# Performance work log

Measured on AMD Instinct MI355X. Metric: run time of the kernel, lower is better.

## Reference

```python
import jax, jax.numpy as jnp
import numpy as np

D_MODEL = 512
N_HEADS = 8
B, T = 2, 2048
EPS = 1e-6


def _phi(x):
    # ELU feature map: elu(x) + 1 (always positive)
    return jax.nn.elu(x) + 1.0


def setup_inputs() -> dict:
    key = jax.random.key(0)
    ks = jax.random.split(key, 9)
    s = 1.0 / np.sqrt(D_MODEL)
    x = jax.random.normal(ks[0], (B, T, D_MODEL), dtype=jnp.float32)
    Wq = jax.random.uniform(ks[1], (D_MODEL, D_MODEL), jnp.float32, -s, s)
    bq = jax.random.uniform(ks[2], (D_MODEL,), jnp.float32, -s, s)
    Wk = jax.random.uniform(ks[3], (D_MODEL, D_MODEL), jnp.float32, -s, s)
    bk = jax.random.uniform(ks[4], (D_MODEL,), jnp.float32, -s, s)
    Wv = jax.random.uniform(ks[5], (D_MODEL, D_MODEL), jnp.float32, -s, s)
    bv = jax.random.uniform(ks[6], (D_MODEL,), jnp.float32, -s, s)
    Wo = jax.random.uniform(ks[7], (D_MODEL, D_MODEL), jnp.float32, -s, s)
    bo = jax.random.uniform(ks[8], (D_MODEL,), jnp.float32, -s, s)
    return {"x": x, "Wq": Wq, "bq": bq, "Wk": Wk, "bk": bk,
            "Wv": Wv, "bv": bv, "Wo": Wo, "bo": bo}


def reference(x, Wq, bq, Wk, bk, Wv, bv, Wo, bo):
    Bb, Tt, _ = x.shape
    H = N_HEADS
    D = D_MODEL // H

    def heads(W, b):
        # (B,T,d_model) -> (B,H,T,D)
        return (x @ W + b).reshape(Bb, Tt, H, D).transpose(0, 2, 1, 3)

    Q = _phi(heads(Wq, bq))
    K = _phi(heads(Wk, bk))
    V = heads(Wv, bv)

    # Causal linear attention: S_t = sum_{j<=t} phi(K_j) ⊗ V_j, z_t = sum_{j<=t} phi(K_j)
    KV = jnp.einsum('bhtd,bhtm->bhtdm', K, V)   # (B,H,T,D,D)
    S = jnp.cumsum(KV, axis=2)
    z = jnp.cumsum(K, axis=2)
    num = jnp.einsum('bhtd,bhtdm->bhtm', Q, S)  # (B,H,T,D)
    den = jnp.maximum(jnp.einsum('bhtd,bhtd->bht', Q, z), EPS)[..., None]
    out = num / den

    out = out.transpose(0, 2, 1, 3).reshape(Bb, Tt, D_MODEL)
    return out @ Wo + bo
```

## Files before the change

### kernel.cpp

```cpp
#include <hip/hip_runtime.h>
#include <math.h>

#define DM 512
#define NH 8
#define HD 64
#define BB 2
#define TT 2048
#define CHUNK 64
#define NC (TT / CHUNK)
#define BH (BB * NH)
#define ROWS (BB * TT)
#define EPSV 1e-6f

typedef short bf16x8 __attribute__((ext_vector_type(8)));
typedef float f32x4 __attribute__((ext_vector_type(4)));
typedef unsigned short us;

union U4 { us h[4]; uint2 u; };

__device__ __forceinline__ us f2bf(float f) {
    unsigned int u = __float_as_uint(f);
    return (us)((u + 0x7FFFu + ((u >> 16) & 1u)) >> 16);
}
__device__ __forceinline__ float bf2f(us h) {
    return __uint_as_float(((unsigned int)h) << 16);
}
__device__ __forceinline__ void gload16(const void* g, void* l) {
    __builtin_amdgcn_global_load_lds(
        (const __attribute__((address_space(1))) unsigned int*)g,
        (__attribute__((address_space(3))) unsigned int*)l, 16, 0, 0);
}
#define SWZ(r, k) ((k) ^ (((r) & 7) << 3))

__global__ __launch_bounds__(256) void prep(
    const float* __restrict__ x,
    const float* __restrict__ Wq, const float* __restrict__ Wk,
    const float* __restrict__ Wv, const float* __restrict__ Wo,
    us* __restrict__ xb, us* __restrict__ WT)
{
    const int bid = blockIdx.x, tid = threadIdx.x;
    __shared__ float tl[32][33];
    if (bid < 2048) {
        const int i = bid * 256 + tid;
        float4 v = ((const float4*)x)[i];
        U4 o;
        o.h[0] = f2bf(v.x); o.h[1] = f2bf(v.y);
        o.h[2] = f2bf(v.z); o.h[3] = f2bf(v.w);
        ((uint2*)xb)[i] = o.u;
    } else {
        const int b2 = bid - 2048;
        const int which = b2 >> 8, t = b2 & 255;
        const float* W = (which == 0) ? Wq : (which == 1) ? Wk : (which == 2) ? Wv : Wo;
        us* O = WT + (size_t)which * DM * DM;
        const int r0 = (t >> 4) * 32, c0 = (t & 15) * 32;
        const int tr = tid >> 3, tc = tid & 7;
        float4 v = *(const float4*)&W[(size_t)(r0 + tr) * DM + c0 + tc * 4];
        tl[tr][tc * 4 + 0] = v.x; tl[tr][tc * 4 + 1] = v.y;
        tl[tr][tc * 4 + 2] = v.z; tl[tr][tc * 4 + 3] = v.w;
        __syncthreads();
        U4 o;
#pragma unroll
        for (int i = 0; i < 4; ++i) o.h[i] = f2bf(tl[tc * 4 + i][tr]);
        *(uint2*)&O[(size_t)(c0 + tr) * DM + r0 + tc * 4] = o.u;
    }
}

__device__ __forceinline__ void gemm64x128(
    const us* __restrict__ Ag, const us* __restrict__ Bg,
    int r0, int c0, int tid, us* Asl, us* Bsl, f32x4 (&acc)[2][4])
{
    const int lane = tid & 63, wid = tid >> 6;
    const int wr = wid >> 1, wc = wid & 1;
    const int lrow = lane & 15, lk8 = (lane >> 4) * 8;
    const int fa = tid * 8;

    for (int k0 = 0; k0 < DM; k0 += 64) {
        __syncthreads();
#pragma unroll
        for (int i = 0; i < 2; ++i) {
            const int f = fa + i * 2048, row = f >> 6, kp = f & 63;
            gload16(Ag + (size_t)(r0 + row) * DM + k0 + SWZ(row, kp), Asl + f);
        }
#pragma unroll
        for (int i = 0; i < 4; ++i) {
            const int f = fa + i * 2048, row = f >> 6, kp = f & 63;
            gload16(Bg + (size_t)(c0 + row) * DM + k0 + SWZ(row, kp), Bsl + f);
        }
        __syncthreads();
#pragma unroll
        for (int kin = 0; kin < 64; kin += 32) {
            bf16x8 af[2], bfr[4];
#pragma unroll
            for (int mi = 0; mi < 2; ++mi) {
                const int row = wr * 32 + mi * 16 + lrow;
                af[mi] = *(const bf16x8*)&Asl[row * 64 + SWZ(row, kin + lk8)];
            }
#pragma unroll
            for (int ni = 0; ni < 4; ++ni) {
                const int row = wc * 64 + ni * 16 + lrow;
                bfr[ni] = *(const bf16x8*)&Bsl[row * 64 + SWZ(row, kin + lk8)];
            }
#pragma unroll
            for (int mi = 0; mi < 2; ++mi)
#pragma unroll
                for (int ni = 0; ni < 4; ++ni)
                    acc[mi][ni] = __builtin_amdgcn_mfma_f32_16x16x32_bf16(
                        af[mi], bfr[ni], acc[mi][ni], 0, 0, 0);
        }
    }
}

__global__ __launch_bounds__(256) void qkv_mfma(
    const us* __restrict__ xb, const us* __restrict__ WT,
    const float* __restrict__ bq, const float* __restrict__ bk,
    const float* __restrict__ bv,
    us* __restrict__ qn, us* __restrict__ kn,
    us* __restrict__ kt, us* __restrict__ vt)
{
    const int which = blockIdx.z;
    const us* Bg = WT + (size_t)which * DM * DM;
    const float* bias = (which == 0) ? bq : (which == 1) ? bk : bv;

    __shared__ us Asl[64 * 64];
    __shared__ us Bsl[128 * 64];
    f32x4 acc[2][4] = {};
    const int r0 = blockIdx.x * 64, c0 = blockIdx.y * 128;
    const int tid = threadIdx.x;

    gemm64x128(xb, Bg, r0, c0, tid, Asl, Bsl, acc);

    const int lane = tid & 63, wid = tid >> 6;
    const int wr = wid >> 1, wc = wid & 1;
    const int lrow = lane & 15, lr4 = (lane >> 4) * 4;
    const int b = r0 >> 11;

#pragma unroll
    for (int mi = 0; mi < 2; ++mi) {
        const int rowb = r0 + wr * 32 + mi * 16 + lr4;
        const int t0g = rowb & (TT - 1);
#pragma unroll
        for (int ni = 0; ni < 4; ++ni) {
            const int col = c0 + wc * 64 + ni * 16 + lrow;
            const int h = col >> 6, d = col & 63;
            const float bc = bias[col];
            U4 p4;
#pragma unroll
            for (int r = 0; r < 4; ++r) {
                float y = acc[mi][ni][r] + bc;
                if (which < 2) y = (y > 0.f) ? (y + 1.f) : __expf(y);
                const us hb = f2bf(y);
                p4.h[r] = hb;
                if (which == 0)
                    qn[((size_t)(b * NH + h) * TT + t0g + r) * HD + d] = hb;
                else if (which == 1)
                    kn[((size_t)(b * NH + h) * TT + t0g + r) * HD + d] = hb;
            }
            if (which == 1)
                *(uint2*)&kt[((size_t)(b * NH + h) * HD + d) * TT + t0g] = p4.u;
            else if (which == 2)
                *(uint2*)&vt[((size_t)(b * NH + h) * HD + d) * TT + t0g] = p4.u;
        }
    }
}

__global__ __launch_bounds__(256) void out_mfma(
    const us* __restrict__ Ag, const us* __restrict__ WoT,
    const float* __restrict__ bias, float* __restrict__ out)
{
    __shared__ us Asl[64 * 64];
    __shared__ us Bsl[128 * 64];
    f32x4 acc[2][4] = {};
    const int r0 = blockIdx.x * 64, c0 = blockIdx.y * 128;
    const int tid = threadIdx.x;

    gemm64x128(Ag, WoT, r0, c0, tid, Asl, Bsl, acc);

    const int lane = tid & 63, wid = tid >> 6;
    const int wr = wid >> 1, wc = wid & 1;
    const int lrow = lane & 15, lr4 = (lane >> 4) * 4;

#pragma unroll
    for (int mi = 0; mi < 2; ++mi)
#pragma unroll
        for (int ni = 0; ni < 4; ++ni) {
            const int col = c0 + wc * 64 + ni * 16 + lrow;
            const float bc = bias[col];
#pragma unroll
            for (int r = 0; r < 4; ++r) {
                const int row = r0 + wr * 32 + mi * 16 + lr4 + r;
                out[(size_t)row * DM + col] = acc[mi][ni][r] + bc;
            }
        }
}

__global__ __launch_bounds__(256) void chunk_sums(
    const us* __restrict__ kt, const us* __restrict__ vt,
    us* __restrict__ kvc, float* __restrict__ zc)
{
    const int blk = blockIdx.x, bh = blk >> 5, c = blk & 31;
    const int t0 = c * CHUNK;
    __shared__ us Ksl[4096], Vsl[4096];
    __shared__ float partial[4][64];
    const int tid = threadIdx.x;
    const us* ktb = kt + (size_t)bh * HD * TT;
    const us* vtb = vt + (size_t)bh * HD * TT;

#pragma unroll
    for (int i = 0; i < 2; ++i) {
        const int f = tid * 8 + i * 2048, row = f >> 6, kp = f & 63;
        const int kl = SWZ(row, kp);
        gload16(ktb + (size_t)row * TT + t0 + kl, Ksl + f);
        gload16(vtb + (size_t)row * TT + t0 + kl, Vsl + f);
    }
    __syncthreads();

    const int lane = tid & 63, wid = tid >> 6;
    const int wr = wid >> 1, wc = wid & 1;
    const int lrow = lane & 15, lk8 = (lane >> 4) * 8, lr4 = (lane >> 4) * 4;

    f32x4 acc[2][2] = {};
#pragma unroll
    for (int kin = 0; kin < 64; kin += 32) {
        bf16x8 af[2], bfr[2];
#pragma unroll
        for (int mi = 0; mi < 2; ++mi) {
            const int row = wr * 32 + mi * 16 + lrow;
            af[mi] = *(const bf16x8*)&Vsl[row * 64 + SWZ(row, kin + lk8)];
        }
#pragma unroll
        for (int ni = 0; ni < 2; ++ni) {
            const int row = wc * 32 + ni * 16 + lrow;
            bfr[ni] = *(const bf16x8*)&Ksl[row * 64 + SWZ(row, kin + lk8)];
        }
#pragma unroll
        for (int mi = 0; mi < 2; ++mi)
#pragma unroll
            for (int ni = 0; ni < 2; ++ni)
                acc[mi][ni] = __builtin_amdgcn_mfma_f32_16x16x32_bf16(
                    af[mi], bfr[ni], acc[mi][ni], 0, 0, 0);
    }

    us* dst = kvc + (size_t)blk * 4096;
#pragma unroll
    for (int mi = 0; mi < 2; ++mi)
#pragma unroll
        for (int ni = 0; ni < 2; ++ni) {
            const int d2 = wr * 32 + mi * 16 + lr4;
            const int d1 = wc * 32 + ni * 16 + lrow;
#pragma unroll
            for (int r = 0; r < 4; ++r)
                dst[(d2 + r) * 64 + d1] = f2bf(acc[mi][ni][r]);
        }

    {
        const int p = tid >> 6, d = tid & 63;
        float s = 0.f;
#pragma unroll
        for (int j = 0; j < 16; ++j)
            s += bf2f(Ksl[d * 64 + SWZ(d, p * 16 + j)]);
        partial[p][d] = s;
    }
    __syncthreads();
    if (tid < 64)
        zc[(size_t)blk * 64 + tid] =
            partial[0][tid] + partial[1][tid] + partial[2][tid] + partial[3][tid];
}

__global__ __launch_bounds__(256) void scan(
    const us* __restrict__ kvc, const float* __restrict__ zc,
    us* __restrict__ spr, float* __restrict__ zpr)
{
    const int bh = blockIdx.x, seg = blockIdx.y, tid = threadIdx.x;
    if (seg < 8) {
        const int e = seg * 512 + tid * 2;
        float r0 = 0.f, r1 = 0.f;
        for (int c = 0; c < NC; ++c) {
            const size_t off = (size_t)(bh * NC + c) * 4096 + e;
            const unsigned u = *(const unsigned*)(kvc + off);
            const unsigned p = (unsigned)f2bf(r0) | ((unsigned)f2bf(r1) << 16);
            *(unsigned*)(spr + off) = p;
            r0 += bf2f((us)(u & 0xFFFF));
            r1 += bf2f((us)(u >> 16));
        }
    } else if (tid < 64) {
        float run = 0.f;
        for (int c = 0; c < NC; ++c) {
            const size_t off = (size_t)(bh * NC + c) * 64 + tid;
            zpr[off] = run;
            run += zc[off];
        }
    }
}

__global__ __launch_bounds__(256) void chunk_attn(
    const us* __restrict__ qn, const us* __restrict__ kn,
    const us* __restrict__ vt, const us* __restrict__ spr,
    const float* __restrict__ zpr, us* __restrict__ attn)
{
    const int blk = blockIdx.x, bh = blk >> 5, c = blk & 31;
    const int t0 = c * CHUNK;
    __shared__ us Qs[4096], Kns[4096], Vts[4096], Sts[4096], Abf[4096];
    __shared__ float zp[64], den[64], part[4][64];
    const int tid = threadIdx.x;

    const us* qb = qn + ((size_t)bh * TT + t0) * HD;
    const us* kb = kn + ((size_t)bh * TT + t0) * HD;
    const us* vb = vt + (size_t)bh * HD * TT;
    const us* sb = spr + (size_t)blk * 4096;

#pragma unroll
    for (int i = 0; i < 2; ++i) {
        const int f = tid * 8 + i * 2048, row = f >> 6, kp = f & 63;
        const int kl = SWZ(row, kp);
        gload16(qb + (size_t)row * HD + kl, Qs + f);
        gload16(kb + (size_t)row * HD + kl, Kns + f);
        gload16(vb + (size_t)row * TT + t0 + kl, Vts + f);
        gload16(sb + (size_t)row * 64 + kl, Sts + f);
    }
    if (tid < 64) zp[tid] = zpr[(size_t)blk * 64 + tid];
    __syncthreads();

    const int lane = tid & 63, wid = tid >> 6;
    const int wr = wid >> 1, wc = wid & 1;
    const int lrow = lane & 15, lk8 = (lane >> 4) * 8, lr4 = (lane >> 4) * 4;

    f32x4 accs[2][2] = {};
#pragma unroll
    for (int kin = 0; kin < 64; kin += 32) {
        bf16x8 af[2], bfr[2];
#pragma unroll
        for (int mi = 0; mi < 2; ++mi) {
            const int row = wr * 32 + mi * 16 + lrow;
            af[mi] = *(const bf16x8*)&Qs[row * 64 + SWZ(row, kin + lk8)];
        }
#pragma unroll
        for (int ni = 0; ni < 2; ++ni) {
            const int row = wc * 32 + ni * 16 + lrow;
            bfr[ni] = *(const bf16x8*)&Kns[row * 64 + SWZ(row, kin + lk8)];
        }
#pragma unroll
        for (int mi = 0; mi < 2; ++mi)
#pragma unroll
            for (int ni = 0; ni < 2; ++ni)
                accs[mi][ni] = __builtin_amdgcn_mfma_f32_16x16x32_bf16(
                    af[mi], bfr[ni], accs[mi][ni], 0, 0, 0);
    }

#pragma unroll
    for (int mi = 0; mi < 2; ++mi)
#pragma unroll
        for (int ni = 0; ni < 2; ++ni) {
            const int j = wc * 32 + ni * 16 + lrow;
#pragma unroll
            for (int r = 0; r < 4; ++r) {
                const int i = wr * 32 + mi * 16 + lr4 + r;
                const float v = (j <= i) ? accs[mi][ni][r] : 0.f;
                Abf[i * 64 + SWZ(i, j)] = f2bf(v);
            }
        }
    __syncthreads();

    {
        const int p = tid >> 6, i = tid & 63;
        float s = 0.f;
#pragma unroll
        for (int jj = 0; jj < 16; ++jj) {
            const int j = p * 16 + jj;
            s += bf2f(Abf[i * 64 + SWZ(i, j)]);
            s += bf2f(Qs[i * 64 + SWZ(i, j)]) * zp[j];
        }
        part[p][i] = s;
    }
    __syncthreads();
    if (tid < 64)
        den[tid] = fmaxf(part[0][tid] + part[1][tid] + part[2][tid] + part[3][tid], EPSV);
    __syncthreads();

    f32x4 acco[2][2] = {};
#pragma unroll
    for (int kin = 0; kin < 64; kin += 32) {
        bf16x8 af[2], bfr[2], ag[2], bgr[2];
#pragma unroll
        for (int mi = 0; mi < 2; ++mi) {
            const int row = wr * 32 + mi * 16 + lrow;
            af[mi] = *(const bf16x8*)&Abf[row * 64 + SWZ(row, kin + lk8)];
            ag[mi] = *(const bf16x8*)&Qs[row * 64 + SWZ(row, kin + lk8)];
        }
#pragma unroll
        for (int ni = 0; ni < 2; ++ni) {
            const int row = wc * 32 + ni * 16 + lrow;
            bfr[ni] = *(const bf16x8*)&Vts[row * 64 + SWZ(row, kin + lk8)];
            bgr[ni] = *(const bf16x8*)&Sts[row * 64 + SWZ(row, kin + lk8)];
        }
#pragma unroll
        for (int mi = 0; mi < 2; ++mi)
#pragma unroll
            for (int ni = 0; ni < 2; ++ni) {
                acco[mi][ni] = __builtin_amdgcn_mfma_f32_16x16x32_bf16(
                    af[mi], bfr[ni], acco[mi][ni], 0, 0, 0);
                acco[mi][ni] = __builtin_amdgcn_mfma_f32_16x16x32_bf16(
                    ag[mi], bgr[ni], acco[mi][ni], 0, 0, 0);
            }
    }

    const int b = bh >> 3, h = bh & 7;
#pragma unroll
    for (int mi = 0; mi < 2; ++mi)
#pragma unroll
        for (int ni = 0; ni < 2; ++ni) {
            const int d2 = wc * 32 + ni * 16 + lrow;
#pragma unroll
            for (int r = 0; r < 4; ++r) {
                const int i = wr * 32 + mi * 16 + lr4 + r;
                attn[((size_t)b * TT + t0 + i) * DM + h * HD + d2] =
                    f2bf(acco[mi][ni][r] / den[i]);
            }
        }
}

extern "C" void kernel_launch(void* const* d_in, const int* in_sizes, int n_in,
                              void* d_out, int out_size, void* d_ws, size_t ws_size,
                              hipStream_t stream)
{
    const float* x  = (const float*)d_in[0];
    const float* Wq = (const float*)d_in[1];
    const float* bq = (const float*)d_in[2];
    const float* Wk = (const float*)d_in[3];
    const float* bk = (const float*)d_in[4];
    const float* Wv = (const float*)d_in[5];
    const float* bv = (const float*)d_in[6];
    const float* Wo = (const float*)d_in[7];
    const float* bo = (const float*)d_in[8];
    float* out = (float*)d_out;

    const size_t SZ = (size_t)BH * TT * HD;
    us* xb  = (us*)d_ws;
    us* WT  = xb + SZ;
    us* qn  = WT + (size_t)4 * DM * DM;
    us* kn  = qn + SZ;
    us* kt  = kn + SZ;
    us* vt  = kt + SZ;
    us* kvc = vt + SZ;
    us* spr = kvc + SZ;
    float* zc  = (float*)(spr + SZ);
    float* zpr = zc + (size_t)BH * NC * 64;
    us* attn = xb;

    prep<<<3072, 256, 0, stream>>>(x, Wq, Wk, Wv, Wo, xb, WT);
    qkv_mfma<<<dim3(ROWS / 64, DM / 128, 3), 256, 0, stream>>>(
        xb, WT, bq, bk, bv, qn, kn, kt, vt);
    chunk_sums<<<BH * NC, 256, 0, stream>>>(kt, vt, kvc, zc);
    scan<<<dim3(BH, 9), 256, 0, stream>>>(kvc, zc, spr, zpr);
    chunk_attn<<<BH * NC, 256, 0, stream>>>(qn, kn, vt, spr, zpr, attn);
    out_mfma<<<dim3(ROWS / 64, DM / 128), 256, 0, stream>>>(attn, WT + (size_t)3 * DM * DM, bo, out);
}
```

Measured before the change: 48.39 us.

## Double-buffer GEMM LDS tiles and batch scan loads up front

The shared 64x128 bf16 GEMM loop now double-buffers its LDS tiles, so global loads for the next K slice are issued before the MFMAs on the current slice, with one barrier per iteration instead of two. The scan kernel first loads all 32 chunk values into registers, then runs the prefix sum, so loads are no longer serialized behind stores. The cost is twice the LDS per GEMM block (48 KB), which may reduce occupancy, and more registers in scan.

```diff
diff --git a/kernel.cpp b/kernel.cpp
--- a/kernel.cpp
+++ b/kernel.cpp
@@ -65,6 +65,23 @@
     }
 }
 
+__device__ __forceinline__ void stage_tiles(
+    const us* __restrict__ Ag, const us* __restrict__ Bg,
+    int r0, int c0, int k0, int tid, us* As, us* Bs)
+{
+    const int fa = tid * 8;
+#pragma unroll
+    for (int i = 0; i < 2; ++i) {
+        const int f = fa + i * 2048, row = f >> 6, kp = f & 63;
+        gload16(Ag + (size_t)(r0 + row) * DM + k0 + SWZ(row, kp), As + f);
+    }
+#pragma unroll
+    for (int i = 0; i < 4; ++i) {
+        const int f = fa + i * 2048, row = f >> 6, kp = f & 63;
+        gload16(Bg + (size_t)(c0 + row) * DM + k0 + SWZ(row, kp), Bs + f);
+    }
+}
+
 __device__ __forceinline__ void gemm64x128(
     const us* __restrict__ Ag, const us* __restrict__ Bg,
     int r0, int c0, int tid, us* Asl, us* Bsl, f32x4 (&acc)[2][4])
@@ -72,33 +89,28 @@
     const int lane = tid & 63, wid = tid >> 6;
     const int wr = wid >> 1, wc = wid & 1;
     const int lrow = lane & 15, lk8 = (lane >> 4) * 8;
-    const int fa = tid * 8;
-
+
+    stage_tiles(Ag, Bg, r0, c0, 0, tid, Asl, Bsl);
+    __syncthreads();
+    int cur = 0;
     for (int k0 = 0; k0 < DM; k0 += 64) {
-        __syncthreads();
-#pragma unroll
-        for (int i = 0; i < 2; ++i) {
-            const int f = fa + i * 2048, row = f >> 6, kp = f & 63;
-            gload16(Ag + (size_t)(r0 + row) * DM + k0 + SWZ(row, kp), Asl + f);
-        }
-#pragma unroll
-        for (int i = 0; i < 4; ++i) {
-            const int f = fa + i * 2048, row = f >> 6, kp = f & 63;
-            gload16(Bg + (size_t)(c0 + row) * DM + k0 + SWZ(row, kp), Bsl + f);
-        }
-        __syncthreads();
+        if (k0 + 64 < DM)
+            stage_tiles(Ag, Bg, r0, c0, k0 + 64, tid,
+                        Asl + (cur ^ 1) * 4096, Bsl + (cur ^ 1) * 8192);
+        const us* As = Asl + cur * 4096;
+        const us* Bs = Bsl + cur * 8192;
 #pragma unroll
         for (int kin = 0; kin < 64; kin += 32) {
             bf16x8 af[2], bfr[4];
 #pragma unroll
             for (int mi = 0; mi < 2; ++mi) {
                 const int row = wr * 32 + mi * 16 + lrow;
-                af[mi] = *(const bf16x8*)&Asl[row * 64 + SWZ(row, kin + lk8)];
+                af[mi] = *(const bf16x8*)&As[row * 64 + SWZ(row, kin + lk8)];
             }
 #pragma unroll
             for (int ni = 0; ni < 4; ++ni) {
                 const int row = wc * 64 + ni * 16 + lrow;
-                bfr[ni] = *(const bf16x8*)&Bsl[row * 64 + SWZ(row, kin + lk8)];
+                bfr[ni] = *(const bf16x8*)&Bs[row * 64 + SWZ(row, kin + lk8)];
             }
 #pragma unroll
             for (int mi = 0; mi < 2; ++mi)
@@ -107,6 +119,8 @@
                     acc[mi][ni] = __builtin_amdgcn_mfma_f32_16x16x32_bf16(
                         af[mi], bfr[ni], acc[mi][ni], 0, 0, 0);
         }
+        __syncthreads();
+        cur ^= 1;
     }
 }
 
@@ -121,8 +135,8 @@
     const us* Bg = WT + (size_t)which * DM * DM;
     const float* bias = (which == 0) ? bq : (which == 1) ? bk : bv;
 
-    __shared__ us Asl[64 * 64];
-    __shared__ us Bsl[128 * 64];
+    __shared__ us Asl[2 * 4096];
+    __shared__ us Bsl[2 * 8192];
     f32x4 acc[2][4] = {};
     const int r0 = blockIdx.x * 64, c0 = blockIdx.y * 128;
     const int tid = threadIdx.x;
@@ -167,8 +181,8 @@
     const us* __restrict__ Ag, const us* __restrict__ WoT,
     const float* __restrict__ bias, float* __restrict__ out)
 {
-    __shared__ us Asl[64 * 64];
-    __shared__ us Bsl[128 * 64];
+    __shared__ us Asl[2 * 4096];
+    __shared__ us Bsl[2 * 8192];
     f32x4 acc[2][4] = {};
     const int r0 = blockIdx.x * 64, c0 = blockIdx.y * 128;
     const int tid = threadIdx.x;
@@ -273,21 +287,29 @@
     const int bh = blockIdx.x, seg = blockIdx.y, tid = threadIdx.x;
     if (seg < 8) {
         const int e = seg * 512 + tid * 2;
+        const size_t base = (size_t)(bh * NC) * 4096 + e;
+        unsigned u[NC];
+#pragma unroll
+        for (int c = 0; c < NC; ++c)
+            u[c] = *(const unsigned*)(kvc + base + (size_t)c * 4096);
         float r0 = 0.f, r1 = 0.f;
+#pragma unroll
         for (int c = 0; c < NC; ++c) {
-            const size_t off = (size_t)(bh * NC + c) * 4096 + e;
-            const unsigned u = *(const unsigned*)(kvc + off);
             const unsigned p = (unsigned)f2bf(r0) | ((unsigned)f2bf(r1) << 16);
-            *(unsigned*)(spr + off) = p;
-            r0 += bf2f((us)(u & 0xFFFF));
-            r1 += bf2f((us)(u >> 16));
+            *(unsigned*)(spr + base + (size_t)c * 4096) = p;
+            r0 += bf2f((us)(u[c] & 0xFFFF));
+            r1 += bf2f((us)(u[c] >> 16));
         }
     } else if (tid < 64) {
+        const size_t base = (size_t)(bh * NC) * 64 + tid;
+        float zv[NC];
+#pragma unroll
+        for (int c = 0; c < NC; ++c) zv[c] = zc[base + (size_t)c * 64];
         float run = 0.f;
+#pragma unroll
         for (int c = 0; c < NC; ++c) {
-            const size_t off = (size_t)(bh * NC + c) * 64 + tid;
-            zpr[off] = run;
-            run += zc[off];
+            zpr[base + (size_t)c * 64] = run;
+            run += zv[c];
         }
     }
 }
@@ -452,5 +474,6 @@
     chunk_sums<<<BH * NC, 256, 0, stream>>>(kt, vt, kvc, zc);
     scan<<<dim3(BH, 9), 256, 0, stream>>>(kvc, zc, spr, zpr);
     chunk_attn<<<BH * NC, 256, 0, stream>>>(qn, kn, vt, spr, zpr, attn);
-    out_mfma<<<dim3(ROWS / 64, DM / 128), 256, 0, stream>>>(attn, WT + (size_t)3 * DM * DM, bo, out);
-}
+    out_mfma<<<dim3(ROWS / 64, DM / 128), 256, 0, stream>>>(
+        attn, WT + (size_t)3 * DM * DM, bo, out);
+}
```

New measurement: 49.31 us. About the same (+1.9%).
